# Optimization experiments

Measured on AMD Instinct MI355X. Metric: run time of the kernel, lower is better.

## Reference

```python
import jax, jax.numpy as jnp
import numpy as np

N, E = 10000, 30000
D_IN, E_DIM, H1, H2, C = 64, 16, 128, 64, 10


def setup_inputs() -> dict:
    key = jax.random.key(0)
    ks = jax.random.split(key, 12)
    x = jax.random.normal(ks[0], (N, D_IN), dtype=jnp.float32)
    edge_attr = jax.random.normal(ks[1], (E, E_DIM), dtype=jnp.float32)
    edge_index = jax.random.randint(ks[2], (2, E), 0, N, dtype=jnp.int64)
    # linear1: D_IN -> H1
    W1 = jax.random.normal(ks[3], (D_IN, H1), dtype=jnp.float32) / np.sqrt(D_IN)
    b1 = jnp.zeros((H1,), dtype=jnp.float32)
    # edge MLP 1: E_DIM -> H1*H2
    We1 = jax.random.normal(ks[4], (E_DIM, H1 * H2), dtype=jnp.float32) / np.sqrt(E_DIM)
    be1 = jnp.zeros((H1 * H2,), dtype=jnp.float32)
    root1 = jax.random.uniform(ks[5], (H1, H2), dtype=jnp.float32,
                               minval=-1.0 / np.sqrt(H1), maxval=1.0 / np.sqrt(H1))
    bias1 = jnp.zeros((H2,), dtype=jnp.float32)
    # edge MLP 2: E_DIM -> H2*C
    We2 = jax.random.normal(ks[6], (E_DIM, H2 * C), dtype=jnp.float32) / np.sqrt(E_DIM)
    be2 = jnp.zeros((H2 * C,), dtype=jnp.float32)
    root2 = jax.random.uniform(ks[7], (H2, C), dtype=jnp.float32,
                               minval=-1.0 / np.sqrt(H2), maxval=1.0 / np.sqrt(H2))
    bias2 = jnp.zeros((C,), dtype=jnp.float32)
    return {"x": x, "edge_attr": edge_attr, "edge_index": edge_index,
            "W1": W1, "b1": b1, "We1": We1, "be1": be1, "root1": root1, "bias1": bias1,
            "We2": We2, "be2": be2, "root2": root2, "bias2": bias2}


def _nnconv(h, src, dst, edge_attr, We, be, root, bias, c_in, c_out):
    # per-edge weight matrix from edge MLP: [E, c_in, c_out]
    W_e = (edge_attr @ We + be).reshape(-1, c_in, c_out)
    msg = jnp.einsum('ei,eio->eo', h[src], W_e)          # gather + batched matmul
    agg = jax.ops.segment_sum(msg, dst, num_segments=N)   # scatter-add to target nodes
    return agg + h @ root + bias


def reference(x, edge_attr, edge_index, W1, b1, We1, be1, root1, bias1,
              We2, be2, root2, bias2):
    src, dst = edge_index[0], edge_index[1]  # PyG: x_j = x[src], aggregate at dst
    h = jax.nn.relu(x @ W1 + b1)                               # [N, H1]
    h = jax.nn.relu(_nnconv(h, src, dst, edge_attr, We1, be1, root1, bias1, H1, H2))
    z = _nnconv(h, src, dst, edge_attr, We2, be2, root2, bias2, H2, C)
    return jax.nn.log_softmax(z, axis=1)
```

## Files before the change

### kernel.cpp

```cpp
#include <hip/hip_runtime.h>

#define N_NODES 10000
#define N_EDGES 30000
#define DIN     64
#define EDIM    16
#define H1      128
#define H2      64
#define C_OUT   10

typedef __bf16 bfrag __attribute__((ext_vector_type(8)));
typedef float  f32x4 __attribute__((ext_vector_type(4)));
typedef ushort ushort8 __attribute__((ext_vector_type(8)));

__device__ __forceinline__ ushort f2bf(float f) {
    union { float f; unsigned u; } x; x.f = f;
    unsigned r = x.u + 0x7fffu + ((x.u >> 16) & 1u);
    return (ushort)(r >> 16);
}
__device__ __forceinline__ float bf2f(ushort s) {
    union { unsigned u; float f; } x; x.u = ((unsigned)s) << 16;
    return x.f;
}

#define KA_B1   1250
#define KA_B2   (KA_B1 + 576)
#define KA_B3   (KA_B2 + 48)
__global__ __launch_bounds__(256) void kA_prep(
        const float* __restrict__ x, const float* __restrict__ W1,
        const float* __restrict__ b1,
        const float* __restrict__ We1, const float* __restrict__ root1,
        const float* __restrict__ be1,
        const float* __restrict__ We2, const float* __restrict__ be2,
        const float* __restrict__ root2,
        ushort* __restrict__ h_bf, ushort* __restrict__ B1t,
        ushort* __restrict__ B2t) {
    int t = threadIdx.x;
    int bx = blockIdx.x;
    if (bx < KA_B1) {
        __shared__ float w_lds[DIN * H1];
        __shared__ float b_lds[H1];
        __shared__ float x_lds[8][DIN];
        for (int idx = t; idx < DIN * H1 / 4; idx += 256)
            ((float4*)w_lds)[idx] = ((const float4*)W1)[idx];
        if (t < H1) b_lds[t] = b1[t];
        int n0 = bx * 8;
        if (t < 128) {
            int row = t >> 4, c4 = t & 15;
            int n = n0 + row;
            float4 v = make_float4(0.f, 0.f, 0.f, 0.f);
            if (n < N_NODES) v = ((const float4*)(x + (size_t)n * DIN))[c4];
            ((float4*)(x_lds[row]))[c4] = v;
        }
        __syncthreads();
        int nl = t >> 5;
        int o  = (t & 31) * 4;
        int n  = n0 + nl;
        float4 acc = *(const float4*)&b_lds[o];
        #pragma unroll 8
        for (int i = 0; i < DIN; ++i) {
            float xv = x_lds[nl][i];
            float4 w = *(const float4*)&w_lds[i * H1 + o];
            acc.x = fmaf(xv, w.x, acc.x);
            acc.y = fmaf(xv, w.y, acc.y);
            acc.z = fmaf(xv, w.z, acc.z);
            acc.w = fmaf(xv, w.w, acc.w);
        }
        if (n < N_NODES) {
            ushort4 s;
            s.x = f2bf(fmaxf(acc.x, 0.f));
            s.y = f2bf(fmaxf(acc.y, 0.f));
            s.z = f2bf(fmaxf(acc.z, 0.f));
            s.w = f2bf(fmaxf(acc.w, 0.f));
            *(ushort4*)&h_bf[(size_t)n * H1 + o] = s;
        }
    } else if (bx < KA_B2) {
        int idx = (bx - KA_B1) * 256 + t;
        int c = idx >> 7, i = idx & 127;
        float v;
        if (c < 1024) {
            int o = c >> 4, k = c & 15;
            v = We1[(size_t)k * (H1 * H2) + i * 64 + o];
        } else if (c < 1088) v = root1[i * 64 + (c - 1024)];
        else                 v = be1[i * 64 + (c - 1088)];
        B1t[idx] = f2bf(v);
    } else {
        int idx = (bx - KA_B2) * 256 + t;
        int c = idx >> 6, j = idx & 63;
        float v = 0.f;
        if (c < 160) {
            int cc = c >> 4, k = c & 15;
            v = We2[(size_t)k * 640 + j * 10 + cc];
        }
        else if (c < 170) v = be2[j * 10 + (c - 160)];
        else if (c < 180) v = root2[j * 10 + (c - 170)];
        B2t[idx] = f2bf(v);
    }
}

__global__ __launch_bounds__(256) void k3_mfma(
        const ushort* __restrict__ h_bf, const ushort* __restrict__ Bt,
        const float* __restrict__ bias1,
        ushort* __restrict__ G1t, float* __restrict__ agg1,
        float* __restrict__ hb1) {
    int t = threadIdx.x;
    int wave = t >> 6, lane = t & 63;
    int quad = lane >> 4, lrow = lane & 15;
    int yy = blockIdx.y;
    int mx = blockIdx.x;
    int nbase = mx * 128 + wave * 32;
    int ar0 = nbase + lrow;       if (ar0 > N_NODES - 1) ar0 = N_NODES - 1;
    int ar1 = nbase + 16 + lrow;  if (ar1 > N_NODES - 1) ar1 = N_NODES - 1;
    bfrag A0[4], A1[4];
    #pragma unroll
    for (int kc4 = 0; kc4 < 4; ++kc4) {
        A0[kc4] = *reinterpret_cast<const bfrag*>(
            h_bf + (size_t)ar0 * 128 + kc4 * 32 + quad * 8);
        A1[kc4] = *reinterpret_cast<const bfrag*>(
            h_bf + (size_t)ar1 * 128 + kc4 * 32 + quad * 8);
    }
    #pragma unroll
    for (int hy = 0; hy < 3; ++hy) {
        int y = yy * 3 + hy;
        const ushort* bbase = Bt + (size_t)y * 64 * 128;
        f32x4 acc0[4] = {}, acc1[4] = {};
        #pragma unroll
        for (int kc4 = 0; kc4 < 4; ++kc4) {
            #pragma unroll
            for (int ct = 0; ct < 4; ++ct) {
                bfrag b = *reinterpret_cast<const bfrag*>(
                    bbase + (size_t)(ct * 16 + lrow) * 128 + kc4 * 32 + quad * 8);
                acc0[ct] = __builtin_amdgcn_mfma_f32_16x16x32_bf16(A0[kc4], b, acc0[ct], 0, 0, 0);
                acc1[ct] = __builtin_amdgcn_mfma_f32_16x16x32_bf16(A1[kc4], b, acc1[ct], 0, 0, 0);
            }
        }
        #pragma unroll
        for (int half = 0; half < 2; ++half) {
            int rbase = nbase + half * 16 + quad * 4;
            #pragma unroll
            for (int ct = 0; ct < 4; ++ct) {
                int col = ct * 16 + lrow;
                f32x4 a = half ? acc1[ct] : acc0[ct];
                #pragma unroll
                for (int r = 0; r < 4; ++r) {
                    int n = rbase + r;
                    if (n >= N_NODES) continue;
                    float v = a[r];
                    if (y < 16) {
                        G1t[(size_t)n * 1024 + y * 64 + col] = f2bf(v);
                    } else if (y == 16) {
                        agg1[(size_t)n * 64 + col] = v + bias1[col];
                    } else {
                        hb1[(size_t)n * 64 + col] = v;
                    }
                }
            }
        }
    }
}

__global__ __launch_bounds__(256) void k4_edge1(
        const float* __restrict__ ea, const int* __restrict__ src_idx,
        const int* __restrict__ dst_idx, const ushort* __restrict__ G1t,
        const float* __restrict__ hb1, float* __restrict__ agg1) {
    int t = threadIdx.x;
    int e0 = blockIdx.x * 16 + (t >> 6) * 4;
    int o = t & 63;
    int s[4], d[4];
    #pragma unroll
    for (int j = 0; j < 4; ++j) { s[j] = src_idx[e0 + j]; d[j] = dst_idx[e0 + j]; }
    ushort8 g[4][2];
    #pragma unroll
    for (int j = 0; j < 4; ++j) {
        const ushort* gp = G1t + (size_t)s[j] * 1024 + o * 16;
        g[j][0] = *reinterpret_cast<const ushort8*>(gp);
        g[j][1] = *reinterpret_cast<const ushort8*>(gp + 8);
    }
    float m[4];
    #pragma unroll
    for (int j = 0; j < 4; ++j) m[j] = hb1[(size_t)s[j] * 64 + o];
    const float* a = ea + (size_t)e0 * 16;
    #pragma unroll
    for (int j = 0; j < 4; ++j) {
        #pragma unroll
        for (int k = 0; k < 8; ++k)
            m[j] = fmaf(a[j * 16 + k], bf2f(g[j][0][k]), m[j]);
        #pragma unroll
        for (int k = 0; k < 8; ++k)
            m[j] = fmaf(a[j * 16 + 8 + k], bf2f(g[j][1][k]), m[j]);
    }
    #pragma unroll
    for (int j = 0; j < 4; ++j)
        atomicAdd(&agg1[(size_t)d[j] * 64 + o], m[j]);
}

__global__ __launch_bounds__(256) void k56_mfma(
        const float* __restrict__ agg1, const ushort* __restrict__ B2t,
        const float* __restrict__ bias2,
        float* __restrict__ G2t, float* __restrict__ hb2,
        float* __restrict__ agg2) {
    int t = threadIdx.x;
    int wave = t >> 6, lane = t & 63;
    int quad = lane >> 4, lrow = lane & 15;
    int n0 = blockIdx.x * 64 + wave * 16;
    int arow = n0 + lrow; if (arow > N_NODES - 1) arow = N_NODES - 1;
    bfrag A[2];
    #pragma unroll
    for (int kk = 0; kk < 2; ++kk) {
        size_t off = (size_t)arow * 64 + kk * 32 + quad * 8;
        f32x4 p0 = *(const f32x4*)(agg1 + off);
        f32x4 p1 = *(const f32x4*)(agg1 + off + 4);
        bfrag a;
        #pragma unroll
        for (int j = 0; j < 4; ++j) {
            a[j]     = (__bf16)fmaxf(p0[j], 0.f);
            a[j + 4] = (__bf16)fmaxf(p1[j], 0.f);
        }
        A[kk] = a;
    }
    #pragma unroll
    for (int y = 0; y < 3; ++y) {
        f32x4 acc[4] = {};
        #pragma unroll
        for (int kk = 0; kk < 2; ++kk) {
            #pragma unroll
            for (int ct = 0; ct < 4; ++ct) {
                bfrag b = *reinterpret_cast<const bfrag*>(
                    B2t + (size_t)(y * 64 + ct * 16 + lrow) * 64 + kk * 32 + quad * 8);
                acc[ct] = __builtin_amdgcn_mfma_f32_16x16x32_bf16(A[kk], b, acc[ct], 0, 0, 0);
            }
        }
        #pragma unroll
        for (int ct = 0; ct < 4; ++ct) {
            int cg = y * 64 + ct * 16 + lrow;
            #pragma unroll
            for (int r = 0; r < 4; ++r) {
                int n = n0 + quad * 4 + r;
                if (n >= N_NODES) continue;
                float v = acc[ct][r];
                if (cg < 160)      G2t[(size_t)n * 160 + cg] = v;
                else if (cg < 170) hb2[(size_t)n * 10 + (cg - 160)] = v;
                else if (cg < 180) agg2[(size_t)n * 10 + (cg - 170)] = v + bias2[cg - 170];
            }
        }
    }
}

__global__ __launch_bounds__(256) void k7_edge2(
        const float* __restrict__ ea, const int* __restrict__ src_idx,
        const int* __restrict__ dst_idx, const float* __restrict__ G2t,
        const float* __restrict__ hb2, float* __restrict__ agg2) {
    int tid = blockIdx.x * 256 + threadIdx.x;
    if (tid >= N_EDGES * 10) return;
    int e = tid / 10, c = tid - e * 10;
    int s = src_idx[e], d = dst_idx[e];
    float m = hb2[(size_t)s * 10 + c];
    const float* g = G2t + (size_t)s * 160 + c * 16;
    const float* a = ea + (size_t)e * 16;
    f32x4 g0 = *(const f32x4*)g,       g1 = *(const f32x4*)(g + 4);
    f32x4 g2 = *(const f32x4*)(g + 8), g3 = *(const f32x4*)(g + 12);
    f32x4 a0 = *(const f32x4*)a,       a1 = *(const f32x4*)(a + 4);
    f32x4 a2 = *(const f32x4*)(a + 8), a3 = *(const f32x4*)(a + 12);
    #pragma unroll
    for (int k = 0; k < 4; ++k) {
        m = fmaf(a0[k], g0[k], m);
        m = fmaf(a1[k], g1[k], m);
        m = fmaf(a2[k], g2[k], m);
        m = fmaf(a3[k], g3[k], m);
    }
    atomicAdd(&agg2[(size_t)d * 10 + c], m);
}

__global__ void k8_logsoftmax(const float* __restrict__ agg2,
                              float* __restrict__ out) {
    int n = blockIdx.x * blockDim.x + threadIdx.x;
    if (n >= N_NODES) return;
    float z[10]; float m = -1e30f;
    #pragma unroll
    for (int c = 0; c < 10; ++c) {
        z[c] = agg2[(size_t)n * 10 + c];
        m = fmaxf(m, z[c]);
    }
    float s = 0.f;
    #pragma unroll
    for (int c = 0; c < 10; ++c) s += expf(z[c] - m);
    float ls = logf(s);
    #pragma unroll
    for (int c = 0; c < 10; ++c) out[(size_t)n * 10 + c] = z[c] - m - ls;
}

extern "C" void kernel_launch(void* const* d_in, const int* in_sizes, int n_in,
                              void* d_out, int out_size, void* d_ws, size_t ws_size,
                              hipStream_t stream) {
    const float* x     = (const float*)d_in[0];
    const float* ea    = (const float*)d_in[1];
    const int*   eidx  = (const int*)d_in[2];
    const float* W1    = (const float*)d_in[3];
    const float* b1    = (const float*)d_in[4];
    const float* We1   = (const float*)d_in[5];
    const float* be1   = (const float*)d_in[6];
    const float* root1 = (const float*)d_in[7];
    const float* bias1 = (const float*)d_in[8];
    const float* We2   = (const float*)d_in[9];
    const float* be2   = (const float*)d_in[10];
    const float* root2 = (const float*)d_in[11];
    const float* bias2 = (const float*)d_in[12];
    float* out = (float*)d_out;

    float* ws = (float*)d_ws;
    ushort* h_bf = (ushort*)ws;
    ushort* B1t  = (ushort*)(ws + 640000);
    ushort* B2t  = (ushort*)(ws + 713728);
    ushort* G1t  = (ushort*)(ws + 719872);
    float* hb1  = ws + 719872 + 5120000;
    float* agg1 = hb1  + 640000;
    float* agg2 = agg1 + 640000;
    float* G2t  = agg2 + 100000;
    float* hb2  = G2t  + 1600000;

    kA_prep<<<KA_B3, 256, 0, stream>>>(x, W1, b1, We1, root1, be1, We2, be2, root2,
                                       h_bf, B1t, B2t);
    k3_mfma<<<dim3(79, 6), 256, 0, stream>>>(h_bf, B1t, bias1, G1t, agg1, hb1);
    k4_edge1<<<1875, 256, 0, stream>>>(ea, eidx, eidx + N_EDGES, G1t, hb1, agg1);
    k56_mfma<<<157, 256, 0, stream>>>(agg1, B2t, bias2, G2t, hb2, agg2);
    k7_edge2<<<1172, 256, 0, stream>>>(ea, eidx, eidx + N_EDGES, G2t, hb2, agg2);
    k8_logsoftmax<<<40, 256, 0, stream>>>(agg2, out);
}
```

Before: 142.2 us.

## Fuse all GNN stages into one cooperative persistent kernel with grid syncs

Combines the prep, the two MFMA GEMMs, the two edge scatter phases and log-softmax into a single cooperative kernel. It launches about three blocks per CU and separates phases with grid.sync plus thread fences. The aim is to remove the launch gaps and tail bubbles between the six separate kernels. The per-wave edge granularity of the first edge phase also drops from 4 to 2 edges, and the fallback multi-kernel path is kept in case the cooperative launch fails. The trade-offs are the cost of five grid-wide barriers and low utilisation in the smaller phases, such as the 157-item second GEMM, while the large LDS footprint stays resident throughout.

```diff
diff --git a/kernel.cpp b/kernel.cpp
--- a/kernel.cpp
+++ b/kernel.cpp
@@ -1,4 +1,7 @@
 #include <hip/hip_runtime.h>
+#include <hip/hip_cooperative_groups.h>
+
+namespace cg = cooperative_groups;
 
 #define N_NODES 10000
 #define N_EDGES 30000
@@ -20,6 +23,280 @@
 __device__ __forceinline__ float bf2f(ushort s) {
     union { unsigned u; float f; } x; x.u = ((unsigned)s) << 16;
     return x.f;
+}
+
+__global__ __launch_bounds__(256, 3) void fused(
+        const float* __restrict__ x, const float* __restrict__ ea,
+        const int* __restrict__ src_idx, const int* __restrict__ dst_idx,
+        const float* __restrict__ W1, const float* __restrict__ b1,
+        const float* __restrict__ We1, const float* __restrict__ be1,
+        const float* __restrict__ root1, const float* __restrict__ bias1,
+        const float* __restrict__ We2, const float* __restrict__ be2,
+        const float* __restrict__ root2, const float* __restrict__ bias2,
+        ushort* __restrict__ h_bf, ushort* __restrict__ B1t,
+        ushort* __restrict__ B2t, ushort* __restrict__ G1t,
+        float* __restrict__ hb1, float* __restrict__ agg1,
+        float* __restrict__ agg2, float* __restrict__ G2t,
+        float* __restrict__ hb2, float* __restrict__ out) {
+    cg::grid_group grid = cg::this_grid();
+    const int t   = threadIdx.x;
+    const int bid = blockIdx.x;
+    const int nb  = gridDim.x;
+
+    {
+        __shared__ float w_lds[DIN * H1];
+        __shared__ float b_lds[H1];
+        __shared__ float x_lds[8][DIN];
+        for (int idx = t; idx < DIN * H1 / 4; idx += 256)
+            ((float4*)w_lds)[idx] = ((const float4*)W1)[idx];
+        if (t < H1) b_lds[t] = b1[t];
+        for (int idx = bid * 256 + t; idx < 1152 * 128; idx += nb * 256) {
+            int c = idx >> 7, i = idx & 127;
+            float v;
+            if (c < 1024) {
+                int o = c >> 4, k = c & 15;
+                v = We1[(size_t)k * (H1 * H2) + i * 64 + o];
+            } else if (c < 1088) v = root1[i * 64 + (c - 1024)];
+            else                 v = be1[i * 64 + (c - 1088)];
+            B1t[idx] = f2bf(v);
+        }
+        for (int idx = bid * 256 + t; idx < 192 * 64; idx += nb * 256) {
+            int c = idx >> 6, j = idx & 63;
+            float v = 0.f;
+            if (c < 160) {
+                int cc = c >> 4, k = c & 15;
+                v = We2[(size_t)k * 640 + j * 10 + cc];
+            }
+            else if (c < 170) v = be2[j * 10 + (c - 160)];
+            else if (c < 180) v = root2[j * 10 + (c - 170)];
+            B2t[idx] = f2bf(v);
+        }
+        __syncthreads();
+        for (int wb = bid; wb < 1250; wb += nb) {
+            int n0 = wb * 8;
+            if (t < 128) {
+                int row = t >> 4, c4 = t & 15;
+                int n = n0 + row;
+                float4 v = make_float4(0.f, 0.f, 0.f, 0.f);
+                if (n < N_NODES) v = ((const float4*)(x + (size_t)n * DIN))[c4];
+                ((float4*)(x_lds[row]))[c4] = v;
+            }
+            __syncthreads();
+            int nl = t >> 5;
+            int o  = (t & 31) * 4;
+            int n  = n0 + nl;
+            float4 acc = *(const float4*)&b_lds[o];
+            #pragma unroll 8
+            for (int i = 0; i < DIN; ++i) {
+                float xv = x_lds[nl][i];
+                float4 w = *(const float4*)&w_lds[i * H1 + o];
+                acc.x = fmaf(xv, w.x, acc.x);
+                acc.y = fmaf(xv, w.y, acc.y);
+                acc.z = fmaf(xv, w.z, acc.z);
+                acc.w = fmaf(xv, w.w, acc.w);
+            }
+            if (n < N_NODES) {
+                ushort4 s;
+                s.x = f2bf(fmaxf(acc.x, 0.f));
+                s.y = f2bf(fmaxf(acc.y, 0.f));
+                s.z = f2bf(fmaxf(acc.z, 0.f));
+                s.w = f2bf(fmaxf(acc.w, 0.f));
+                *(ushort4*)&h_bf[(size_t)n * H1 + o] = s;
+            }
+            __syncthreads();
+        }
+    }
+    __threadfence();
+    grid.sync();
+    __threadfence();
+
+    {
+        int wave = t >> 6, lane = t & 63;
+        int quad = lane >> 4, lrow = lane & 15;
+        for (int item = bid; item < 79 * 6; item += nb) {
+            int mx = item % 79, yy = item / 79;
+            int nbase = mx * 128 + wave * 32;
+            int ar0 = nbase + lrow;       if (ar0 > N_NODES - 1) ar0 = N_NODES - 1;
+            int ar1 = nbase + 16 + lrow;  if (ar1 > N_NODES - 1) ar1 = N_NODES - 1;
+            bfrag A0[4], A1[4];
+            #pragma unroll
+            for (int kc4 = 0; kc4 < 4; ++kc4) {
+                A0[kc4] = *reinterpret_cast<const bfrag*>(
+                    h_bf + (size_t)ar0 * 128 + kc4 * 32 + quad * 8);
+                A1[kc4] = *reinterpret_cast<const bfrag*>(
+                    h_bf + (size_t)ar1 * 128 + kc4 * 32 + quad * 8);
+            }
+            #pragma unroll
+            for (int hy = 0; hy < 3; ++hy) {
+                int y = yy * 3 + hy;
+                const ushort* bbase = B1t + (size_t)y * 64 * 128;
+                f32x4 acc0[4] = {}, acc1[4] = {};
+                #pragma unroll
+                for (int kc4 = 0; kc4 < 4; ++kc4) {
+                    #pragma unroll
+                    for (int ct = 0; ct < 4; ++ct) {
+                        bfrag b = *reinterpret_cast<const bfrag*>(
+                            bbase + (size_t)(ct * 16 + lrow) * 128 + kc4 * 32 + quad * 8);
+                        acc0[ct] = __builtin_amdgcn_mfma_f32_16x16x32_bf16(A0[kc4], b, acc0[ct], 0, 0, 0);
+                        acc1[ct] = __builtin_amdgcn_mfma_f32_16x16x32_bf16(A1[kc4], b, acc1[ct], 0, 0, 0);
+                    }
+                }
+                #pragma unroll
+                for (int half = 0; half < 2; ++half) {
+                    int rbase = nbase + half * 16 + quad * 4;
+                    #pragma unroll
+                    for (int ct = 0; ct < 4; ++ct) {
+                        int col = ct * 16 + lrow;
+                        f32x4 a = half ? acc1[ct] : acc0[ct];
+                        #pragma unroll
+                        for (int r = 0; r < 4; ++r) {
+                            int n = rbase + r;
+                            if (n >= N_NODES) continue;
+                            float v = a[r];
+                            if (y < 16) {
+                                G1t[(size_t)n * 1024 + y * 64 + col] = f2bf(v);
+                            } else if (y == 16) {
+                                agg1[(size_t)n * 64 + col] = v + bias1[col];
+                            } else {
+                                hb1[(size_t)n * 64 + col] = v;
+                            }
+                        }
+                    }
+                }
+            }
+        }
+    }
+    __threadfence();
+    grid.sync();
+    __threadfence();
+
+    {
+        int o = t & 63;
+        for (int grp = bid; grp < 3750; grp += nb) {
+            int e0 = grp * 8 + (t >> 6) * 2;
+            int s0 = src_idx[e0],     d0 = dst_idx[e0];
+            int s1 = src_idx[e0 + 1], d1 = dst_idx[e0 + 1];
+            const ushort* g0p = G1t + (size_t)s0 * 1024 + o * 16;
+            const ushort* g1p = G1t + (size_t)s1 * 1024 + o * 16;
+            ushort8 ga0 = *reinterpret_cast<const ushort8*>(g0p);
+            ushort8 ga1 = *reinterpret_cast<const ushort8*>(g0p + 8);
+            ushort8 gb0 = *reinterpret_cast<const ushort8*>(g1p);
+            ushort8 gb1 = *reinterpret_cast<const ushort8*>(g1p + 8);
+            float m0 = hb1[(size_t)s0 * 64 + o];
+            float m1 = hb1[(size_t)s1 * 64 + o];
+            const float* a0 = ea + (size_t)e0 * 16;
+            const float* a1 = a0 + 16;
+            #pragma unroll
+            for (int k = 0; k < 8; ++k) {
+                m0 = fmaf(a0[k], bf2f(ga0[k]), m0);
+                m1 = fmaf(a1[k], bf2f(gb0[k]), m1);
+            }
+            #pragma unroll
+            for (int k = 0; k < 8; ++k) {
+                m0 = fmaf(a0[k + 8], bf2f(ga1[k]), m0);
+                m1 = fmaf(a1[k + 8], bf2f(gb1[k]), m1);
+            }
+            atomicAdd(&agg1[(size_t)d0 * 64 + o], m0);
+            atomicAdd(&agg1[(size_t)d1 * 64 + o], m1);
+        }
+    }
+    __threadfence();
+    grid.sync();
+    __threadfence();
+
+    {
+        int wave = t >> 6, lane = t & 63;
+        int quad = lane >> 4, lrow = lane & 15;
+        for (int item = bid; item < 157; item += nb) {
+            int n0 = item * 64 + wave * 16;
+            int arow = n0 + lrow; if (arow > N_NODES - 1) arow = N_NODES - 1;
+            bfrag A[2];
+            #pragma unroll
+            for (int kk = 0; kk < 2; ++kk) {
+                size_t off = (size_t)arow * 64 + kk * 32 + quad * 8;
+                f32x4 p0 = *(const f32x4*)(agg1 + off);
+                f32x4 p1 = *(const f32x4*)(agg1 + off + 4);
+                bfrag a;
+                #pragma unroll
+                for (int j = 0; j < 4; ++j) {
+                    a[j]     = (__bf16)fmaxf(p0[j], 0.f);
+                    a[j + 4] = (__bf16)fmaxf(p1[j], 0.f);
+                }
+                A[kk] = a;
+            }
+            #pragma unroll
+            for (int y = 0; y < 3; ++y) {
+                f32x4 acc[4] = {};
+                #pragma unroll
+                for (int kk = 0; kk < 2; ++kk) {
+                    #pragma unroll
+                    for (int ct = 0; ct < 4; ++ct) {
+                        bfrag b = *reinterpret_cast<const bfrag*>(
+                            B2t + (size_t)(y * 64 + ct * 16 + lrow) * 64 + kk * 32 + quad * 8);
+                        acc[ct] = __builtin_amdgcn_mfma_f32_16x16x32_bf16(A[kk], b, acc[ct], 0, 0, 0);
+                    }
+                }
+                #pragma unroll
+                for (int ct = 0; ct < 4; ++ct) {
+                    int cg = y * 64 + ct * 16 + lrow;
+                    #pragma unroll
+                    for (int r = 0; r < 4; ++r) {
+                        int n = n0 + quad * 4 + r;
+                        if (n >= N_NODES) continue;
+                        float v = acc[ct][r];
+                        if (cg < 160)      G2t[(size_t)n * 160 + cg] = v;
+                        else if (cg < 170) hb2[(size_t)n * 10 + (cg - 160)] = v;
+                        else if (cg < 180) agg2[(size_t)n * 10 + (cg - 170)] = v + bias2[cg - 170];
+                    }
+                }
+            }
+        }
+    }
+    __threadfence();
+    grid.sync();
+    __threadfence();
+
+    {
+        for (int tid = bid * 256 + t; tid < N_EDGES * 10; tid += nb * 256) {
+            int e = tid / 10, c = tid - e * 10;
+            int s = src_idx[e], d = dst_idx[e];
+            float m = hb2[(size_t)s * 10 + c];
+            const float* g = G2t + (size_t)s * 160 + c * 16;
+            const float* a = ea + (size_t)e * 16;
+            f32x4 g0 = *(const f32x4*)g,       g1 = *(const f32x4*)(g + 4);
+            f32x4 g2 = *(const f32x4*)(g + 8), g3 = *(const f32x4*)(g + 12);
+            f32x4 a0 = *(const f32x4*)a,       a1 = *(const f32x4*)(a + 4);
+            f32x4 a2 = *(const f32x4*)(a + 8), a3 = *(const f32x4*)(a + 12);
+            #pragma unroll
+            for (int k = 0; k < 4; ++k) {
+                m = fmaf(a0[k], g0[k], m);
+                m = fmaf(a1[k], g1[k], m);
+                m = fmaf(a2[k], g2[k], m);
+                m = fmaf(a3[k], g3[k], m);
+            }
+            atomicAdd(&agg2[(size_t)d * 10 + c], m);
+        }
+    }
+    __threadfence();
+    grid.sync();
+    __threadfence();
+
+    {
+        for (int n = bid * 256 + t; n < N_NODES; n += nb * 256) {
+            float z[10]; float m = -1e30f;
+            #pragma unroll
+            for (int c = 0; c < 10; ++c) {
+                z[c] = agg2[(size_t)n * 10 + c];
+                m = fmaxf(m, z[c]);
+            }
+            float s = 0.f;
+            #pragma unroll
+            for (int c = 0; c < 10; ++c) s += expf(z[c] - m);
+            float ls = logf(s);
+            #pragma unroll
+            for (int c = 0; c < 10; ++c) out[(size_t)n * 10 + c] = z[c] - m - ls;
+        }
+    }
 }
 
 #define KA_B1   1250
@@ -163,34 +440,32 @@
         const int* __restrict__ dst_idx, const ushort* __restrict__ G1t,
         const float* __restrict__ hb1, float* __restrict__ agg1) {
     int t = threadIdx.x;
-    int e0 = blockIdx.x * 16 + (t >> 6) * 4;
+    int e0 = blockIdx.x * 8 + (t >> 6) * 2;
     int o = t & 63;
-    int s[4], d[4];
-    #pragma unroll
-    for (int j = 0; j < 4; ++j) { s[j] = src_idx[e0 + j]; d[j] = dst_idx[e0 + j]; }
-    ushort8 g[4][2];
-    #pragma unroll
-    for (int j = 0; j < 4; ++j) {
-        const ushort* gp = G1t + (size_t)s[j] * 1024 + o * 16;
-        g[j][0] = *reinterpret_cast<const ushort8*>(gp);
-        g[j][1] = *reinterpret_cast<const ushort8*>(gp + 8);
-    }
-    float m[4];
-    #pragma unroll
-    for (int j = 0; j < 4; ++j) m[j] = hb1[(size_t)s[j] * 64 + o];
-    const float* a = ea + (size_t)e0 * 16;
-    #pragma unroll
-    for (int j = 0; j < 4; ++j) {
-        #pragma unroll
-        for (int k = 0; k < 8; ++k)
-            m[j] = fmaf(a[j * 16 + k], bf2f(g[j][0][k]), m[j]);
-        #pragma unroll
-        for (int k = 0; k < 8; ++k)
-            m[j] = fmaf(a[j * 16 + 8 + k], bf2f(g[j][1][k]), m[j]);
-    }
-    #pragma unroll
-    for (int j = 0; j < 4; ++j)
-        atomicAdd(&agg1[(size_t)d[j] * 64 + o], m[j]);
+    int s0 = src_idx[e0],     d0 = dst_idx[e0];
+    int s1 = src_idx[e0 + 1], d1 = dst_idx[e0 + 1];
+    const ushort* g0p = G1t + (size_t)s0 * 1024 + o * 16;
+    const ushort* g1p = G1t + (size_t)s1 * 1024 + o * 16;
+    ushort8 ga0 = *reinterpret_cast<const ushort8*>(g0p);
+    ushort8 ga1 = *reinterpret_cast<const ushort8*>(g0p + 8);
+    ushort8 gb0 = *reinterpret_cast<const ushort8*>(g1p);
+    ushort8 gb1 = *reinterpret_cast<const ushort8*>(g1p + 8);
+    float m0 = hb1[(size_t)s0 * 64 + o];
+    float m1 = hb1[(size_t)s1 * 64 + o];
+    const float* a0 = ea + (size_t)e0 * 16;
+    const float* a1 = a0 + 16;
+    #pragma unroll
+    for (int k = 0; k < 8; ++k) {
+        m0 = fmaf(a0[k], bf2f(ga0[k]), m0);
+        m1 = fmaf(a1[k], bf2f(gb0[k]), m1);
+    }
+    #pragma unroll
+    for (int k = 0; k < 8; ++k) {
+        m0 = fmaf(a0[k + 8], bf2f(ga1[k]), m0);
+        m1 = fmaf(a1[k + 8], bf2f(gb1[k]), m1);
+    }
+    atomicAdd(&agg1[(size_t)d0 * 64 + o], m0);
+    atomicAdd(&agg1[(size_t)d1 * 64 + o], m1);
 }
 
 __global__ __launch_bounds__(256) void k56_mfma(
@@ -305,6 +580,8 @@
     const float* root2 = (const float*)d_in[11];
     const float* bias2 = (const float*)d_in[12];
     float* out = (float*)d_out;
+    const int* src_idx = eidx;
+    const int* dst_idx = eidx + N_EDGES;
 
     float* ws = (float*)d_ws;
     ushort* h_bf = (ushort*)ws;
@@ -317,11 +594,47 @@
     float* G2t  = agg2 + 100000;
     float* hb2  = G2t  + 1600000;
 
-    kA_prep<<<KA_B3, 256, 0, stream>>>(x, W1, b1, We1, root1, be1, We2, be2, root2,
-                                       h_bf, B1t, B2t);
-    k3_mfma<<<dim3(79, 6), 256, 0, stream>>>(h_bf, B1t, bias1, G1t, agg1, hb1);
-    k4_edge1<<<1875, 256, 0, stream>>>(ea, eidx, eidx + N_EDGES, G1t, hb1, agg1);
-    k56_mfma<<<157, 256, 0, stream>>>(agg1, B2t, bias2, G2t, hb2, agg2);
-    k7_edge2<<<1172, 256, 0, stream>>>(ea, eidx, eidx + N_EDGES, G2t, hb2, agg2);
-    k8_logsoftmax<<<40, 256, 0, stream>>>(agg2, out);
-}
+    static int coop_nb = -2;
+    if (coop_nb == -2) {
+        int occ = 0;
+        hipError_t e = hipOccupancyMaxActiveBlocksPerMultiprocessor(
+            &occ, (const void*)fused, 256, 0);
+        if (e == hipSuccess && occ > 0) {
+            int per_cu = occ > 3 ? 3 : occ;
+            coop_nb = per_cu * 256;
+        } else {
+            coop_nb = -1;
+        }
+    }
+
+    bool launched = false;
+    if (coop_nb > 0) {
+        void* args[] = {
+            (void*)&x, (void*)&ea, (void*)&src_idx, (void*)&dst_idx,
+            (void*)&W1, (void*)&b1, (void*)&We1, (void*)&be1,
+            (void*)&root1, (void*)&bias1, (void*)&We2, (void*)&be2,
+            (void*)&root2, (void*)&bias2,
+            (void*)&h_bf, (void*)&B1t, (void*)&B2t, (void*)&G1t,
+            (void*)&hb1, (void*)&agg1, (void*)&agg2, (void*)&G2t,
+            (void*)&hb2, (void*)&out
+        };
+        hipError_t e = hipLaunchCooperativeKernel((const void*)fused,
+                                                  dim3(coop_nb), dim3(256),
+                                                  args, 0, stream);
+        if (e == hipSuccess) {
+            launched = true;
+        } else {
+            coop_nb = -1;
+        }
+    }
+
+    if (!launched) {
+        kA_prep<<<KA_B3, 256, 0, stream>>>(x, W1, b1, We1, root1, be1,
+                                           We2, be2, root2, h_bf, B1t, B2t);
+        k3_mfma<<<dim3(79, 6), 256, 0, stream>>>(h_bf, B1t, bias1, G1t, agg1, hb1);
+        k4_edge1<<<3750, 256, 0, stream>>>(ea, src_idx, dst_idx, G1t, hb1, agg1);
+        k56_mfma<<<157, 256, 0, stream>>>(agg1, B2t, bias2, G2t, hb2, agg2);
+        k7_edge2<<<1172, 256, 0, stream>>>(ea, src_idx, dst_idx, G2t, hb2, agg2);
+        k8_logsoftmax<<<40, 256, 0, stream>>>(agg2, out);
+    }
+}
```

Result: slower. 510.3 us (+258.8%).
